# Optimization experiments

Hardware: AMD Instinct MI355X
Metric: run time of the kernel (lower is better)

Reference implementation:

```python
import jax, jax.numpy as jnp
import numpy as np

NEG_SLOPE = 0.01
LN_EPS = 1e-5

def _layer_norm(h, g, b):
    mu = jnp.mean(h, axis=-1, keepdims=True)
    var = jnp.mean(jnp.square(h - mu), axis=-1, keepdims=True)
    return (h - mu) * jax.lax.rsqrt(var + LN_EPS) * g + b

def _mlp(h, Wa, ba, g, be, Wb, bb):
    h = h @ Wa + ba
    h = jnp.where(h >= 0, h, NEG_SLOPE * h)  # LeakyReLU
    h = _layer_norm(h, g, be)
    return h @ Wb + bb

def setup_inputs() -> dict:
    N, E = 50000, 800000
    DN, DE, DG, DO = 128, 64, 32, 128
    key = jax.random.key(0)
    ks = jax.random.split(key, 16)
    def lin(k, fan_in, fan_out):
        lim = 1.0 / np.sqrt(fan_in)
        k1, k2 = jax.random.split(k)
        W = jax.random.uniform(k1, (fan_in, fan_out), jnp.float32, -lim, lim)
        b = jax.random.uniform(k2, (fan_out,), jnp.float32, -lim, lim)
        return W, b
    W1a, b1a = lin(ks[0], DN + DE + DG, DO)
    W1b, b1b = lin(ks[1], DO, DO)
    W2a, b2a = lin(ks[2], DN + DO, DO)
    W2b, b2b = lin(ks[3], DO, DO)
    return {
        "x": jax.random.normal(ks[4], (N, DN), jnp.float32),
        "edge_index": jax.random.randint(ks[5], (2, E), 0, N, jnp.int32),
        "edge_attr": jax.random.normal(ks[6], (E, DE), jnp.float32),
        "u": jax.random.normal(ks[7], (DG,), jnp.float32),
        "batch": jnp.zeros((N,), jnp.int32),
        "W1a": W1a, "b1a": b1a,
        "g1": jnp.ones((DO,), jnp.float32), "be1": jnp.zeros((DO,), jnp.float32),
        "W1b": W1b, "b1b": b1b,
        "W2a": W2a, "b2a": b2a,
        "g2": jnp.ones((DO,), jnp.float32), "be2": jnp.zeros((DO,), jnp.float32),
        "W2b": W2b, "b2b": b2b,
    }

def reference(x, edge_index, edge_attr, u, batch,
              W1a, b1a, g1, be1, W1b, b1b,
              W2a, b2a, g2, be2, W2b, b2b):
    src, dest = edge_index[0], edge_index[1]
    E = edge_attr.shape[0]
    N = x.shape[0]
    # gather + concat: [E, DN+DE+DG]
    h = jnp.concatenate([x[src], edge_attr,
                         jnp.broadcast_to(u[None, :], (E, u.shape[0]))], axis=1)
    h = _mlp(h, W1a, b1a, g1, be1, W1b, b1b)
    # scatter_mean by dest
    sums = jax.ops.segment_sum(h, dest, num_segments=N)
    cnt = jax.ops.segment_sum(jnp.ones((E,), h.dtype), dest, num_segments=N)
    agg = sums / jnp.maximum(cnt, 1.0)[:, None]
    return _mlp(jnp.concatenate([x, agg], axis=1), W2a, b2a, g2, be2, W2b, b2b)
```

## Files before the change

### kernel.cpp

```cpp
#include <hip/hip_runtime.h>
#include <hip/hip_fp16.h>
#include <hip/hip_bf16.h>

constexpr int DN = 128, DE = 64, DG = 32, DO = 128;
constexpr int K1 = DN + DE + DG;
constexpr float NEG_SLOPE = 0.01f;
constexpr float LN_EPS = 1e-5f;

constexpr int EPB = 128;
constexpr int NB  = 64;
constexpr int T_LD = 136;

typedef __attribute__((ext_vector_type(8))) short bf16x8;
typedef __attribute__((ext_vector_type(4))) float f32x4;

__device__ inline unsigned short f2bf(float f) {
    unsigned u = __builtin_bit_cast(unsigned, f);
    u += 0x7FFFu + ((u >> 16) & 1u);
    return (unsigned short)(u >> 16);
}

__device__ inline bf16x8 pk8(float4 p, float4 q) {
    bf16x8 r;
    r[0] = (short)f2bf(p.x); r[1] = (short)f2bf(p.y);
    r[2] = (short)f2bf(p.z); r[3] = (short)f2bf(p.w);
    r[4] = (short)f2bf(q.x); r[5] = (short)f2bf(q.y);
    r[6] = (short)f2bf(q.z); r[7] = (short)f2bf(q.w);
    return r;
}

__global__ void wprep_kernel(const float* __restrict__ W1a,
                             const float* __restrict__ W1b,
                             const float* __restrict__ W2a,
                             const float* __restrict__ W2b,
                             unsigned short* __restrict__ tab) {
    int idx = blockIdx.x * 256 + threadIdx.x;
    if (idx >= 23 * 512) return;
    int slabset = idx >> 9;
    int rem = idx & 511;
    const float* W; int sl;
    if (slabset < 7)       { W = W1a; sl = slabset; }
    else if (slabset < 11) { W = W1b; sl = slabset - 7; }
    else if (slabset < 19) { W = W2a; sl = slabset - 11; }
    else                   { W = W2b; sl = slabset - 19; }
    int nt = rem >> 6, lane = rem & 63;
    int quad = lane >> 4, l15 = lane & 15;
    int n = nt * 16 + l15;
    int k0 = sl * 32 + quad * 8;
    union { ushort4 u4[2]; unsigned short s[8]; } o;
#pragma unroll
    for (int j = 0; j < 8; ++j) o.s[j] = f2bf(W[(long)(k0 + j) * DO + n]);
    *(ushort4*)&tab[(long)idx * 8]     = o.u4[0];
    *(ushort4*)&tab[(long)idx * 8 + 4] = o.u4[1];
}

__global__ __launch_bounds__(256) void edge_kernel(
    const float* __restrict__ x, const int* __restrict__ edge_index,
    const float* __restrict__ edge_attr, const float* __restrict__ u,
    const unsigned short* __restrict__ tab,
    const float* __restrict__ b1a, const float* __restrict__ g1,
    const float* __restrict__ be1,
    __half* __restrict__ sums, float* __restrict__ cnt, int E)
{
    __shared__ int s_src[EPB], s_dst[EPB];

    const int tid = threadIdx.x, lane = tid & 63, wave = tid >> 6;
    const int l15 = lane & 15, quad = lane >> 4;
    const int ebase = blockIdx.x * EPB;
    const int evalid = min(EPB, E - ebase);

    if (tid < EPB) {
        int e = ebase + tid; bool v = tid < evalid;
        s_src[tid] = v ? edge_index[e] : 0;
        s_dst[tid] = v ? edge_index[E + e] : 0;
    }
    __syncthreads();

    const int r0 = wave * 32 + l15, r1 = r0 + 16;
    const long xs0 = (long)s_src[r0] * DN;
    const long xs1 = (long)s_src[r1] * DN;
    const long er0 = (long)min(ebase + r0, E - 1) * DE;
    const long er1 = (long)min(ebase + r1, E - 1) * DE;
    const bf16x8* tW1a = (const bf16x8*)tab;
    const int kq = quad * 8;

    f32x4 acc[2][8];
#pragma unroll
    for (int mt = 0; mt < 2; ++mt)
#pragma unroll
        for (int nt = 0; nt < 8; ++nt) acc[mt][nt] = (f32x4){0.f, 0.f, 0.f, 0.f};

#pragma unroll
    for (int ks = 0; ks < 7; ++ks) {
        float4 p0, q0, p1, q1;
        if (ks < 4) {
            const float* b0 = &x[xs0 + ks * 32 + kq];
            const float* b1 = &x[xs1 + ks * 32 + kq];
            p0 = *(const float4*)b0; q0 = *(const float4*)(b0 + 4);
            p1 = *(const float4*)b1; q1 = *(const float4*)(b1 + 4);
        } else if (ks < 6) {
            int c = ks * 32 - DN + kq;
            const float* b0 = &edge_attr[er0 + c];
            const float* b1 = &edge_attr[er1 + c];
            p0 = *(const float4*)b0; q0 = *(const float4*)(b0 + 4);
            p1 = *(const float4*)b1; q1 = *(const float4*)(b1 + 4);
        } else {
            p0 = *(const float4*)&u[kq]; q0 = *(const float4*)&u[kq + 4];
            p1 = p0; q1 = q0;
        }
        bf16x8 a0 = pk8(p0, q0);
        bf16x8 a1 = pk8(p1, q1);
#pragma unroll
        for (int nt = 0; nt < 8; ++nt) {
            bf16x8 b = tW1a[(ks * 8 + nt) * 64 + lane];
            acc[0][nt] = __builtin_amdgcn_mfma_f32_16x16x32_bf16(a0, b, acc[0][nt], 0, 0, 0);
            acc[1][nt] = __builtin_amdgcn_mfma_f32_16x16x32_bf16(a1, b, acc[1][nt], 0, 0, 0);
        }
    }

    float ba[8], gg[8], bb[8];
#pragma unroll
    for (int nt = 0; nt < 8; ++nt) {
        int col = nt * 16 + l15;
        ba[nt] = b1a[col]; gg[nt] = g1[col]; bb[nt] = be1[col];
    }
#pragma unroll
    for (int mt = 0; mt < 2; ++mt) {
#pragma unroll
        for (int r = 0; r < 4; ++r) {
            float v[8];
            float s = 0.f, q = 0.f;
#pragma unroll
            for (int nt = 0; nt < 8; ++nt) {
                float t = acc[mt][nt][r] + ba[nt];
                t = (t >= 0.f) ? t : NEG_SLOPE * t;
                v[nt] = t; s += t; q += t * t;
            }
#pragma unroll
            for (int off = 1; off < 16; off <<= 1) {
                s += __shfl_xor(s, off, 64);
                q += __shfl_xor(q, off, 64);
            }
            float mu  = s * (1.f / DO);
            float var = q * (1.f / DO) - mu * mu;
            float rs  = rsqrtf(var + LN_EPS);
            int lrow = wave * 32 + mt * 16 + quad * 4 + r;
            bool doat = (lrow < evalid);
            long base = (long)s_dst[lrow] * DO;
#pragma unroll
            for (int nt = 0; nt < 8; ++nt) {
                float h  = (v[nt] - mu) * rs * gg[nt] + bb[nt];
                float hp = __shfl_xor(h, 1, 64);
                if (doat && ((l15 & 1) == 0)) {
                    __half2 pv = __halves2half2(__float2half_rn(h),
                                                __float2half_rn(hp));
                    unsafeAtomicAdd((__half2*)&sums[base + nt * 16 + l15], pv);
                }
            }
        }
    }
    if (tid < evalid) atomicAdd(&cnt[s_dst[tid]], 1.0f);
}

__global__ __launch_bounds__(256) void node_kernel(
    const float* __restrict__ x, const __half* __restrict__ sums,
    const float* __restrict__ cnt, const unsigned short* __restrict__ tab,
    const float* __restrict__ b1b, const float* __restrict__ b2a,
    const float* __restrict__ g2, const float* __restrict__ be2,
    const float* __restrict__ b2b,
    float* __restrict__ out, int N)
{
    __shared__ unsigned short s_t[4][16 * T_LD];

    const int tid = threadIdx.x, lane = tid & 63, wave = tid >> 6;
    const int l15 = lane & 15, quad = lane >> 4;
    const int nbase = blockIdx.x * NB;

    const bf16x8* tW1b = (const bf16x8*)tab + 7 * 512;
    const bf16x8* tW2a = (const bf16x8*)tab + 11 * 512;
    const bf16x8* tW2b = (const bf16x8*)tab + 19 * 512;

    const int nodeA = min(nbase + wave * 16 + l15, N - 1);
    const float invc = 1.f / fmaxf(cnt[nodeA], 1.f);
    const int kq = quad * 8;

    f32x4 acc[8];

#pragma unroll
    for (int nt = 0; nt < 8; ++nt) acc[nt] = (f32x4){0.f, 0.f, 0.f, 0.f};
#pragma unroll
    for (int ks = 0; ks < 4; ++ks) {
        const __half2* sp = (const __half2*)(sums + (long)nodeA * DO + ks * 32 + kq);
        float2 f0 = __half22float2(sp[0]);
        float2 f1 = __half22float2(sp[1]);
        float2 f2 = __half22float2(sp[2]);
        float2 f3 = __half22float2(sp[3]);
        float4 p = {f0.x * invc, f0.y * invc, f1.x * invc, f1.y * invc};
        float4 q = {f2.x * invc, f2.y * invc, f3.x * invc, f3.y * invc};
        bf16x8 a = pk8(p, q);
#pragma unroll
        for (int nt = 0; nt < 8; ++nt) {
            bf16x8 b = tW1b[(ks * 8 + nt) * 64 + lane];
            acc[nt] = __builtin_amdgcn_mfma_f32_16x16x32_bf16(a, b, acc[nt], 0, 0, 0);
        }
    }
    {
#pragma unroll
        for (int reg = 0; reg < 4; ++reg) {
            int lrow = quad * 4 + reg;
            int nodeC = nbase + wave * 16 + lrow;
            float cf = (nodeC < N && cnt[min(nodeC, N - 1)] > 0.f) ? 1.f : 0.f;
#pragma unroll
            for (int nt = 0; nt < 8; ++nt) {
                float v = acc[nt][reg] + cf * b1b[nt * 16 + l15];
                s_t[wave][lrow * T_LD + nt * 16 + l15] = f2bf(v);
            }
        }
    }

#pragma unroll
    for (int nt = 0; nt < 8; ++nt) acc[nt] = (f32x4){0.f, 0.f, 0.f, 0.f};
#pragma unroll
    for (int ks = 0; ks < 8; ++ks) {
        bf16x8 a;
        if (ks < 4) {
            const float* b0 = &x[(long)nodeA * DN + ks * 32 + kq];
            a = pk8(*(const float4*)b0, *(const float4*)(b0 + 4));
        } else {
            a = *(const bf16x8*)&s_t[wave][l15 * T_LD + (ks - 4) * 32 + kq];
        }
#pragma unroll
        for (int nt = 0; nt < 8; ++nt) {
            bf16x8 b = tW2a[(ks * 8 + nt) * 64 + lane];
            acc[nt] = __builtin_amdgcn_mfma_f32_16x16x32_bf16(a, b, acc[nt], 0, 0, 0);
        }
    }
    {
        float ba[8], gg[8], bb[8];
#pragma unroll
        for (int nt = 0; nt < 8; ++nt) {
            int col = nt * 16 + l15;
            ba[nt] = b2a[col]; gg[nt] = g2[col]; bb[nt] = be2[col];
        }
#pragma unroll
        for (int reg = 0; reg < 4; ++reg) {
            float v[8];
            float s = 0.f, q = 0.f;
#pragma unroll
            for (int nt = 0; nt < 8; ++nt) {
                float t = acc[nt][reg] + ba[nt];
                t = (t >= 0.f) ? t : NEG_SLOPE * t;
                v[nt] = t; s += t; q += t * t;
            }
#pragma unroll
            for (int off = 1; off < 16; off <<= 1) {
                s += __shfl_xor(s, off, 64);
                q += __shfl_xor(q, off, 64);
            }
            float mu  = s * (1.f / DO);
            float var = q * (1.f / DO) - mu * mu;
            float rs  = rsqrtf(var + LN_EPS);
            int lrow = quad * 4 + reg;
#pragma unroll
            for (int nt = 0; nt < 8; ++nt) {
                float h = (v[nt] - mu) * rs * gg[nt] + bb[nt];
                s_t[wave][lrow * T_LD + nt * 16 + l15] = f2bf(h);
            }
        }
    }

#pragma unroll
    for (int nt = 0; nt < 8; ++nt) acc[nt] = (f32x4){0.f, 0.f, 0.f, 0.f};
#pragma unroll
    for (int ks = 0; ks < 4; ++ks) {
        bf16x8 a = *(const bf16x8*)&s_t[wave][l15 * T_LD + ks * 32 + kq];
#pragma unroll
        for (int nt = 0; nt < 8; ++nt) {
            bf16x8 b = tW2b[(ks * 8 + nt) * 64 + lane];
            acc[nt] = __builtin_amdgcn_mfma_f32_16x16x32_bf16(a, b, acc[nt], 0, 0, 0);
        }
    }
    {
#pragma unroll
        for (int reg = 0; reg < 4; ++reg) {
            int nodeC = nbase + wave * 16 + quad * 4 + reg;
            if (nodeC < N) {
                long base = (long)nodeC * DO;
#pragma unroll
                for (int nt = 0; nt < 8; ++nt)
                    out[base + nt * 16 + l15] = acc[nt][reg] + b2b[nt * 16 + l15];
            }
        }
    }
}

extern "C" void kernel_launch(void* const* d_in, const int* in_sizes, int n_in,
                              void* d_out, int out_size, void* d_ws, size_t ws_size,
                              hipStream_t stream)
{
    const float* x          = (const float*)d_in[0];
    const int*   edge_index = (const int*)d_in[1];
    const float* edge_attr  = (const float*)d_in[2];
    const float* u          = (const float*)d_in[3];
    const float* W1a = (const float*)d_in[5];
    const float* b1a = (const float*)d_in[6];
    const float* g1  = (const float*)d_in[7];
    const float* be1 = (const float*)d_in[8];
    const float* W1b = (const float*)d_in[9];
    const float* b1b = (const float*)d_in[10];
    const float* W2a = (const float*)d_in[11];
    const float* b2a = (const float*)d_in[12];
    const float* g2  = (const float*)d_in[13];
    const float* be2 = (const float*)d_in[14];
    const float* W2b = (const float*)d_in[15];
    const float* b2b = (const float*)d_in[16];

    const int N = in_sizes[0] / DN;
    const int E = in_sizes[2] / DE;
    float* out  = (float*)d_out;

    __half* sums = (__half*)d_ws;
    float*  cnt  = (float*)(sums + (size_t)N * DO);
    size_t tab_off = (size_t)N * DO * sizeof(__half) + (size_t)N * sizeof(float);
    tab_off = (tab_off + 15) & ~(size_t)15;
    unsigned short* tab = (unsigned short*)((char*)d_ws + tab_off);

    (void)hipMemsetAsync(d_ws, 0,
                         (size_t)N * DO * sizeof(__half) + (size_t)N * sizeof(float),
                         stream);

    wprep_kernel<<<(23 * 512 + 255) / 256, 256, 0, stream>>>(W1a, W1b, W2a, W2b, tab);

    const int eblocks = (E + EPB - 1) / EPB;
    edge_kernel<<<eblocks, 256, 0, stream>>>(
        x, edge_index, edge_attr, u, tab, b1a, g1, be1, sums, cnt, E);

    const int nblocks = (N + NB - 1) / NB;
    node_kernel<<<nblocks, 256, 0, stream>>>(
        x, sums, cnt, tab, b1b, b2a, g2, be2, b2b, out, N);
}
```

Before: 713.2 us.

## Sort edges by destination, pre-reduce in LDS, fold W1b into W2a

Adds a counting sort of edges by destination (histogram, single-block scan, scatter). The edge kernel processes the sorted edges, stages the per-edge MLP outputs in shared memory, and adds up runs with the same destination before issuing fp32 atomics. This cuts the number of global half2 atomic adds, and node counts now come from the CSR offsets. The second linear layer of the edge MLP is folded algebraically into the node MLP (Wc = W1b·W2a_bottom, plus a precomputed bias term), which removes one GEMM from the node kernel. The trade-offs are extra sort passes, scattered edge_attr reads by edge id, and fp32 sums held in the output buffer.

```diff
diff --git a/kernel.cpp b/kernel.cpp
--- a/kernel.cpp
+++ b/kernel.cpp
@@ -10,6 +10,7 @@
 constexpr int EPB = 128;
 constexpr int NB  = 64;
 constexpr int T_LD = 136;
+constexpr int H_LD = 132;
 
 typedef __attribute__((ext_vector_type(8))) short bf16x8;
 typedef __attribute__((ext_vector_type(4))) float f32x4;
@@ -33,36 +34,119 @@
                              const float* __restrict__ W1b,
                              const float* __restrict__ W2a,
                              const float* __restrict__ W2b,
-                             unsigned short* __restrict__ tab) {
+                             const float* __restrict__ b1b,
+                             unsigned short* __restrict__ tab,
+                             float* __restrict__ bc) {
     int idx = blockIdx.x * 256 + threadIdx.x;
-    if (idx >= 23 * 512) return;
+    if (idx >= 19 * 512 + 128) return;
+    if (idx >= 19 * 512) {
+        int n = idx - 19 * 512;
+        float s = 0.f;
+        for (int j = 0; j < DO; ++j) s += b1b[j] * W2a[(long)(DN + j) * DO + n];
+        bc[n] = s;
+        return;
+    }
     int slabset = idx >> 9;
     int rem = idx & 511;
-    const float* W; int sl;
-    if (slabset < 7)       { W = W1a; sl = slabset; }
-    else if (slabset < 11) { W = W1b; sl = slabset - 7; }
-    else if (slabset < 19) { W = W2a; sl = slabset - 11; }
-    else                   { W = W2b; sl = slabset - 19; }
     int nt = rem >> 6, lane = rem & 63;
     int quad = lane >> 4, l15 = lane & 15;
     int n = nt * 16 + l15;
-    int k0 = sl * 32 + quad * 8;
     union { ushort4 u4[2]; unsigned short s[8]; } o;
-#pragma unroll
-    for (int j = 0; j < 8; ++j) o.s[j] = f2bf(W[(long)(k0 + j) * DO + n]);
+    if (slabset < 7) {
+        int k0 = slabset * 32 + quad * 8;
+#pragma unroll
+        for (int j = 0; j < 8; ++j) o.s[j] = f2bf(W1a[(long)(k0 + j) * DO + n]);
+    } else if (slabset < 11) {
+        int k0 = (slabset - 7) * 32 + quad * 8;
+#pragma unroll
+        for (int j = 0; j < 8; ++j) o.s[j] = f2bf(W2a[(long)(k0 + j) * DO + n]);
+    } else if (slabset < 15) {
+        int k0 = (slabset - 11) * 32 + quad * 8;
+        float s[8] = {0.f, 0.f, 0.f, 0.f, 0.f, 0.f, 0.f, 0.f};
+        for (int j2 = 0; j2 < DO; ++j2) {
+            float wa = W2a[(long)(DN + j2) * DO + n];
+#pragma unroll
+            for (int j = 0; j < 8; ++j) s[j] += W1b[(long)(k0 + j) * DO + j2] * wa;
+        }
+#pragma unroll
+        for (int j = 0; j < 8; ++j) o.s[j] = f2bf(s[j]);
+    } else {
+        int k0 = (slabset - 15) * 32 + quad * 8;
+#pragma unroll
+        for (int j = 0; j < 8; ++j) o.s[j] = f2bf(W2b[(long)(k0 + j) * DO + n]);
+    }
     *(ushort4*)&tab[(long)idx * 8]     = o.u4[0];
     *(ushort4*)&tab[(long)idx * 8 + 4] = o.u4[1];
+}
+
+__global__ void hist_kernel(const int* __restrict__ edge_index,
+                            int* __restrict__ counts, int E) {
+    int e = blockIdx.x * 256 + threadIdx.x;
+    if (e < E) atomicAdd(&counts[edge_index[E + e]], 1);
+}
+
+__global__ __launch_bounds__(1024) void scan_kernel(
+    const int* __restrict__ counts, int* __restrict__ offsets,
+    int* __restrict__ cursor, int N) {
+    __shared__ int s_ws[16];
+    __shared__ int s_carry;
+    const int tid = threadIdx.x, lane = tid & 63, wv = tid >> 6;
+    if (tid == 0) s_carry = 0;
+    __syncthreads();
+    for (int base = 0; base < N; base += 1024) {
+        int i = base + tid;
+        int v = (i < N) ? counts[i] : 0;
+        int s = v;
+#pragma unroll
+        for (int off = 1; off < 64; off <<= 1) {
+            int t = __shfl_up(s, off, 64);
+            if (lane >= off) s += t;
+        }
+        if (lane == 63) s_ws[wv] = s;
+        __syncthreads();
+        if (tid < 16) {
+            int w = s_ws[tid];
+#pragma unroll
+            for (int off = 1; off < 16; off <<= 1) {
+                int t = __shfl_up(w, off, 16);
+                if (tid >= off) w += t;
+            }
+            s_ws[tid] = w;
+        }
+        __syncthreads();
+        int carry = s_carry;
+        int woff = (wv == 0) ? 0 : s_ws[wv - 1];
+        int excl = carry + woff + (s - v);
+        if (i < N) { offsets[i] = excl; cursor[i] = excl; }
+        int total = s_ws[15];
+        __syncthreads();
+        if (tid == 0) s_carry = carry + total;
+        __syncthreads();
+    }
+    if (threadIdx.x == 0) offsets[N] = s_carry;
+}
+
+__global__ void scatter_kernel(const int* __restrict__ edge_index,
+                               int* __restrict__ cursor,
+                               int2* __restrict__ sorted, int E) {
+    int e = blockIdx.x * 256 + threadIdx.x;
+    if (e < E) {
+        int d = edge_index[E + e];
+        int pos = atomicAdd(&cursor[d], 1);
+        sorted[pos] = make_int2(e, d);
+    }
 }
 
 __global__ __launch_bounds__(256) void edge_kernel(
     const float* __restrict__ x, const int* __restrict__ edge_index,
     const float* __restrict__ edge_attr, const float* __restrict__ u,
-    const unsigned short* __restrict__ tab,
+    const int2* __restrict__ sorted, const unsigned short* __restrict__ tab,
     const float* __restrict__ b1a, const float* __restrict__ g1,
     const float* __restrict__ be1,
-    __half* __restrict__ sums, float* __restrict__ cnt, int E)
+    float* __restrict__ sums, int E)
 {
-    __shared__ int s_src[EPB], s_dst[EPB];
+    __shared__ int s_src[EPB], s_eid[EPB], s_dst[EPB];
+    __shared__ alignas(16) __half s_h[EPB * H_LD];
 
     const int tid = threadIdx.x, lane = tid & 63, wave = tid >> 6;
     const int l15 = lane & 15, quad = lane >> 4;
@@ -70,17 +154,19 @@
     const int evalid = min(EPB, E - ebase);
 
     if (tid < EPB) {
-        int e = ebase + tid; bool v = tid < evalid;
-        s_src[tid] = v ? edge_index[e] : 0;
-        s_dst[tid] = v ? edge_index[E + e] : 0;
+        bool v = tid < evalid;
+        int2 ed = v ? sorted[ebase + tid] : make_int2(0, 0);
+        s_eid[tid] = ed.x;
+        s_dst[tid] = ed.y;
+        s_src[tid] = edge_index[ed.x];
     }
     __syncthreads();
 
     const int r0 = wave * 32 + l15, r1 = r0 + 16;
     const long xs0 = (long)s_src[r0] * DN;
     const long xs1 = (long)s_src[r1] * DN;
-    const long er0 = (long)min(ebase + r0, E - 1) * DE;
-    const long er1 = (long)min(ebase + r1, E - 1) * DE;
+    const long er0 = (long)s_eid[r0] * DE;
+    const long er1 = (long)s_eid[r1] * DE;
     const bf16x8* tW1a = (const bf16x8*)tab;
     const int kq = quad * 8;
 
@@ -145,29 +231,44 @@
             float var = q * (1.f / DO) - mu * mu;
             float rs  = rsqrtf(var + LN_EPS);
             int lrow = wave * 32 + mt * 16 + quad * 4 + r;
-            bool doat = (lrow < evalid);
-            long base = (long)s_dst[lrow] * DO;
 #pragma unroll
             for (int nt = 0; nt < 8; ++nt) {
                 float h  = (v[nt] - mu) * rs * gg[nt] + bb[nt];
                 float hp = __shfl_xor(h, 1, 64);
-                if (doat && ((l15 & 1) == 0)) {
-                    __half2 pv = __halves2half2(__float2half_rn(h),
-                                                __float2half_rn(hp));
-                    unsafeAtomicAdd((__half2*)&sums[base + nt * 16 + l15], pv);
+                if ((l15 & 1) == 0) {
+                    *(__half2*)&s_h[lrow * H_LD + nt * 16 + l15] =
+                        __halves2half2(__float2half_rn(h), __float2half_rn(hp));
                 }
             }
         }
     }
-    if (tid < evalid) atomicAdd(&cnt[s_dst[tid]], 1.0f);
+    __syncthreads();
+
+    {
+        const int d = tid & 127, g = tid >> 7;
+        int e0 = g * 64, e1 = min(e0 + 64, evalid);
+        if (e0 < e1) {
+            float accv = 0.f;
+            int cur = s_dst[e0];
+            for (int e = e0; e < e1; ++e) {
+                int dd = s_dst[e];
+                if (dd != cur) {
+                    atomicAdd(&sums[(long)cur * DO + d], accv);
+                    accv = 0.f; cur = dd;
+                }
+                accv += __half2float(s_h[e * H_LD + d]);
+            }
+            atomicAdd(&sums[(long)cur * DO + d], accv);
+        }
+    }
 }
 
 __global__ __launch_bounds__(256) void node_kernel(
-    const float* __restrict__ x, const __half* __restrict__ sums,
-    const float* __restrict__ cnt, const unsigned short* __restrict__ tab,
-    const float* __restrict__ b1b, const float* __restrict__ b2a,
-    const float* __restrict__ g2, const float* __restrict__ be2,
-    const float* __restrict__ b2b,
+    const float* __restrict__ x, const float* __restrict__ sums,
+    const int* __restrict__ offsets, const unsigned short* __restrict__ tab,
+    const float* __restrict__ bc,
+    const float* __restrict__ b2a, const float* __restrict__ g2,
+    const float* __restrict__ be2, const float* __restrict__ b2b,
     float* __restrict__ out, int N)
 {
     __shared__ unsigned short s_t[4][16 * T_LD];
@@ -176,47 +277,16 @@
     const int l15 = lane & 15, quad = lane >> 4;
     const int nbase = blockIdx.x * NB;
 
-    const bf16x8* tW1b = (const bf16x8*)tab + 7 * 512;
-    const bf16x8* tW2a = (const bf16x8*)tab + 11 * 512;
-    const bf16x8* tW2b = (const bf16x8*)tab + 19 * 512;
+    const bf16x8* tW2aT = (const bf16x8*)tab + 7 * 512;
+    const bf16x8* tWc   = (const bf16x8*)tab + 11 * 512;
+    const bf16x8* tW2b  = (const bf16x8*)tab + 15 * 512;
 
     const int nodeA = min(nbase + wave * 16 + l15, N - 1);
-    const float invc = 1.f / fmaxf(cnt[nodeA], 1.f);
+    const int cntA  = offsets[nodeA + 1] - offsets[nodeA];
+    const float invc = 1.f / fmaxf((float)cntA, 1.f);
     const int kq = quad * 8;
 
     f32x4 acc[8];
-
-#pragma unroll
-    for (int nt = 0; nt < 8; ++nt) acc[nt] = (f32x4){0.f, 0.f, 0.f, 0.f};
-#pragma unroll
-    for (int ks = 0; ks < 4; ++ks) {
-        const __half2* sp = (const __half2*)(sums + (long)nodeA * DO + ks * 32 + kq);
-        float2 f0 = __half22float2(sp[0]);
-        float2 f1 = __half22float2(sp[1]);
-        float2 f2 = __half22float2(sp[2]);
-        float2 f3 = __half22float2(sp[3]);
-        float4 p = {f0.x * invc, f0.y * invc, f1.x * invc, f1.y * invc};
-        float4 q = {f2.x * invc, f2.y * invc, f3.x * invc, f3.y * invc};
-        bf16x8 a = pk8(p, q);
-#pragma unroll
-        for (int nt = 0; nt < 8; ++nt) {
-            bf16x8 b = tW1b[(ks * 8 + nt) * 64 + lane];
-            acc[nt] = __builtin_amdgcn_mfma_f32_16x16x32_bf16(a, b, acc[nt], 0, 0, 0);
-        }
-    }
-    {
-#pragma unroll
-        for (int reg = 0; reg < 4; ++reg) {
-            int lrow = quad * 4 + reg;
-            int nodeC = nbase + wave * 16 + lrow;
-            float cf = (nodeC < N && cnt[min(nodeC, N - 1)] > 0.f) ? 1.f : 0.f;
-#pragma unroll
-            for (int nt = 0; nt < 8; ++nt) {
-                float v = acc[nt][reg] + cf * b1b[nt * 16 + l15];
-                s_t[wave][lrow * T_LD + nt * 16 + l15] = f2bf(v);
-            }
-        }
-    }
 
 #pragma unroll
     for (int nt = 0; nt < 8; ++nt) acc[nt] = (f32x4){0.f, 0.f, 0.f, 0.f};
@@ -227,28 +297,38 @@
             const float* b0 = &x[(long)nodeA * DN + ks * 32 + kq];
             a = pk8(*(const float4*)b0, *(const float4*)(b0 + 4));
         } else {
-            a = *(const bf16x8*)&s_t[wave][l15 * T_LD + (ks - 4) * 32 + kq];
-        }
+            const float* sp = &sums[(long)nodeA * DO + (ks - 4) * 32 + kq];
+            float4 p = *(const float4*)sp;
+            float4 q = *(const float4*)(sp + 4);
+            p.x *= invc; p.y *= invc; p.z *= invc; p.w *= invc;
+            q.x *= invc; q.y *= invc; q.z *= invc; q.w *= invc;
+            a = pk8(p, q);
+        }
+        const bf16x8* tB = (ks < 4) ? tW2aT : tWc;
+        const int kk = (ks < 4) ? ks : ks - 4;
 #pragma unroll
         for (int nt = 0; nt < 8; ++nt) {
-            bf16x8 b = tW2a[(ks * 8 + nt) * 64 + lane];
+            bf16x8 b = tB[(kk * 8 + nt) * 64 + lane];
             acc[nt] = __builtin_amdgcn_mfma_f32_16x16x32_bf16(a, b, acc[nt], 0, 0, 0);
         }
     }
     {
-        float ba[8], gg[8], bb[8];
+        float ba[8], gg[8], bb[8], bcv[8];
 #pragma unroll
         for (int nt = 0; nt < 8; ++nt) {
             int col = nt * 16 + l15;
-            ba[nt] = b2a[col]; gg[nt] = g2[col]; bb[nt] = be2[col];
+            ba[nt] = b2a[col]; gg[nt] = g2[col]; bb[nt] = be2[col]; bcv[nt] = bc[col];
         }
 #pragma unroll
         for (int reg = 0; reg < 4; ++reg) {
+            int nodeC = nbase + wave * 16 + quad * 4 + reg;
+            int cc = (nodeC < N) ? (offsets[nodeC + 1] - offsets[nodeC]) : 0;
+            float cf = (cc > 0) ? 1.f : 0.f;
             float v[8];
             float s = 0.f, q = 0.f;
 #pragma unroll
             for (int nt = 0; nt < 8; ++nt) {
-                float t = acc[nt][reg] + ba[nt];
+                float t = acc[nt][reg] + ba[nt] + cf * bcv[nt];
                 t = (t >= 0.f) ? t : NEG_SLOPE * t;
                 v[nt] = t; s += t; q += t * t;
             }
@@ -319,23 +399,31 @@
     const int E = in_sizes[2] / DE;
     float* out  = (float*)d_out;
 
-    __half* sums = (__half*)d_ws;
-    float*  cnt  = (float*)(sums + (size_t)N * DO);
-    size_t tab_off = (size_t)N * DO * sizeof(__half) + (size_t)N * sizeof(float);
-    tab_off = (tab_off + 15) & ~(size_t)15;
-    unsigned short* tab = (unsigned short*)((char*)d_ws + tab_off);
-
-    (void)hipMemsetAsync(d_ws, 0,
-                         (size_t)N * DO * sizeof(__half) + (size_t)N * sizeof(float),
-                         stream);
-
-    wprep_kernel<<<(23 * 512 + 255) / 256, 256, 0, stream>>>(W1a, W1b, W2a, W2b, tab);
+    char* p = (char*)d_ws;
+    int2* sorted = (int2*)p;                      p += (size_t)E * sizeof(int2);
+    unsigned short* tab = (unsigned short*)p;     p += (size_t)19 * 512 * 8 * sizeof(unsigned short);
+    float* bc = (float*)p;                        p += 128 * sizeof(float);
+    int* counts = (int*)p;                        p += (size_t)N * sizeof(int);
+    int* offsets = (int*)p;                       p += (size_t)(N + 1) * sizeof(int);
+    p = (char*)(((uintptr_t)p + 15) & ~(uintptr_t)15);
+    int* cursor = (int*)p;                        p += (size_t)N * sizeof(int);
+    float* sums = (float*)d_out;
+
+    (void)hipMemsetAsync(counts, 0, (size_t)N * sizeof(int), stream);
+    (void)hipMemsetAsync(d_out, 0, (size_t)N * DO * sizeof(float), stream);
+
+    wprep_kernel<<<(19 * 512 + 128 + 255) / 256, 256, 0, stream>>>(
+        W1a, W1b, W2a, W2b, b1b, tab, bc);
+
+    hist_kernel<<<(E + 255) / 256, 256, 0, stream>>>(edge_index, counts, E);
+    scan_kernel<<<1, 1024, 0, stream>>>(counts, offsets, cursor, N);
+    scatter_kernel<<<(E + 255) / 256, 256, 0, stream>>>(edge_index, cursor, sorted, E);
 
     const int eblocks = (E + EPB - 1) / EPB;
     edge_kernel<<<eblocks, 256, 0, stream>>>(
-        x, edge_index, edge_attr, u, tab, b1a, g1, be1, sums, cnt, E);
+        x, edge_index, edge_attr, u, sorted, tab, b1a, g1, be1, sums, E);
 
     const int nblocks = (N + NB - 1) / NB;
     node_kernel<<<nblocks, 256, 0, stream>>>(
-        x, sums, cnt, tab, b1b, b2a, g2, be2, b2b, out, N);
-}
+        x, sums, offsets, tab, bc, b2a, g2, be2, b2b, out, N);
+}
```

Result: slower. 806.2 us (+13.0%).
